# Optimization experiments

Measured on AMD Instinct MI355X. Metric: run time of the kernel, lower is better.

## Reference

```python
import jax, jax.numpy as jnp
import numpy as np


def _conv1d(x, w, b):
    # x: [N, C_in, L], w: [C_out, C_in, K], padding=1 (SAME for K=3)
    y = jax.lax.conv_general_dilated(
        x, w, window_strides=(1,), padding=[(1, 1)],
        dimension_numbers=('NCH', 'OIH', 'NCH'))
    return y + b[None, :, None]


def _pharse_shift(I, r):
    # Faithful vectorized form of the original scalar loop:
    #   New[i, 0, j] = I[i, j % r, j // r];  all other output channels stay zero.
    a, b, c = I.shape
    row0 = jnp.transpose(I[:, :r, :], (0, 2, 1)).reshape(a, c * r)  # interleave channels
    New = jnp.zeros((a, b // r, c * r), dtype=I.dtype)
    return New.at[:, 0, :].set(row0)


def setup_inputs() -> dict:
    key = jax.random.key(0)
    k1, k2, k3, k4, k5 = jax.random.split(key, 5)
    B, C, L = 32, 64, 16384
    x = jax.random.normal(k1, (B, C, L), dtype=jnp.float32)
    # Conv1d(channels, channels, 3) params, PyTorch-style uniform init scale
    s1 = 1.0 / np.sqrt(C * 3)
    w1 = jax.random.uniform(k2, (C, C, 3), minval=-s1, maxval=s1, dtype=jnp.float32)
    b1 = jax.random.uniform(k3, (C,), minval=-s1, maxval=s1, dtype=jnp.float32)
    # Conv1d(channels, 4, 3) params (up_block22)
    w2 = jax.random.uniform(k4, (4, C, 3), minval=-s1, maxval=s1, dtype=jnp.float32)
    b2 = jax.random.uniform(k5, (4,), minval=-s1, maxval=s1, dtype=jnp.float32)
    return {"x": x, "w1": w1, "b1": b1, "w2": w2, "b2": b2, "sc": 4}


def reference(x, w1, b1, w2, b2, sc):
    assert sc in (2, 4)
    h = jax.nn.relu(_conv1d(x, w1, b1))   # up_block1: Conv1d(C,C,3)+ReLU
    h = jax.nn.relu(_conv1d(h, w2, b2))   # up_block22: Conv1d(C,4,3)+ReLU  [B,4,L]
    return _pharse_shift(h, sc)           # [B, 4//sc, L*sc]
```

## Files before the change

### kernel.cpp

```cpp
#include <hip/hip_runtime.h>
#include <hip/hip_bf16.h>


#define CC 64
#define LL 16384
#define NBATCH 32
#define TL 128
#define NTILE 128
#define XROWS 146
#define PITCH 128

typedef short short8 __attribute__((ext_vector_type(8)));
typedef float f32x4 __attribute__((ext_vector_type(4)));

__device__ __forceinline__ unsigned pk2(float a, float b) {
    unsigned short lo = __builtin_bit_cast(unsigned short, __float2bfloat16(a));
    unsigned short hi = __builtin_bit_cast(unsigned short, __float2bfloat16(b));
    return (unsigned)lo | ((unsigned)hi << 16);
}

__global__ void repack_weights(const float* __restrict__ w1,
                               const float* __restrict__ w2,
                               unsigned short* __restrict__ wp) {
    int i = blockIdx.x * 256 + threadIdx.x;
    if (i < 12288) {
        int kk = i >> 12;
        int rem = i & 4095;
        int co = rem >> 6;
        int ci = rem & 63;
        wp[i] = __builtin_bit_cast(unsigned short, __float2bfloat16(w1[(co * 64 + ci) * 3 + kk]));
    }
    if (i < 3072) {
        int kk = i >> 10;
        int rem = i & 1023;
        int oc = rem >> 6;
        int ci = rem & 63;
        float v = (oc < 4) ? w2[(oc * 64 + ci) * 3 + kk] : 0.0f;
        wp[12288 + i] = __builtin_bit_cast(unsigned short, __float2bfloat16(v));
    }
}

__global__ __launch_bounds__(256, 4)
void fused_upsample_mfma(const float* __restrict__ x,
                         const float* __restrict__ b1,
                         const float* __restrict__ b2,
                         const unsigned short* __restrict__ wp,
                         float* __restrict__ out) {
    __shared__ __align__(16) char lds[(XROWS + 2 + 144) * PITCH];
    char* const xs = lds;
    char* const hs = lds + (XROWS + 2) * PITCH;

    const int bid = blockIdx.x;
    const int swz = (bid & 7) * 512 + (bid >> 3);
    const int t   = swz & (NTILE - 1);
    const int bb  = swz >> 7;

    const int tid  = threadIdx.x;
    const int lane = tid & 63;
    const int wave = tid >> 6;
    const int lr   = lane & 15;
    const int lg   = lane >> 4;

    {
        const int sc  = tid & 15;
        const int scg = tid >> 4;
        const long base0 = (long)(bb * CC + scg * 4) * LL;
        const int g0 = t * TL - 2;
        const bool interior = (t > 0) && (t < NTILE - 1);

        if (interior) {
            #pragma unroll
            for (int it = 0; it < 5; ++it) {
                int r = it * 32 + sc * 2;
                if (it < 4 || r < XROWS) {
                    float2 v0 = *(const float2*)(x + base0 + g0 + r);
                    float2 v1 = *(const float2*)(x + base0 + LL + g0 + r);
                    float2 v2 = *(const float2*)(x + base0 + 2 * LL + g0 + r);
                    float2 v3 = *(const float2*)(x + base0 + 3 * LL + g0 + r);
                    int byteA = (r * PITCH + scg * 8) ^ ((r & 7) << 4);
                    int byteB = ((r + 1) * PITCH + scg * 8) ^ (((r + 1) & 7) << 4);
                    *(uint2*)(xs + byteA) = make_uint2(pk2(v0.x, v1.x), pk2(v2.x, v3.x));
                    *(uint2*)(xs + byteB) = make_uint2(pk2(v0.y, v1.y), pk2(v2.y, v3.y));
                }
            }
        } else {
            #pragma unroll
            for (int it = 0; it < 5; ++it) {
                int r = it * 32 + sc * 2;
                if (it < 4 || r < XROWS) {
                    int ga = g0 + r, gb = g0 + r + 1;
                    bool oa = (unsigned)ga < (unsigned)LL;
                    bool ob = (unsigned)gb < (unsigned)LL;
                    float2 v[4];
                    #pragma unroll
                    for (int u = 0; u < 4; ++u) {
                        v[u].x = oa ? x[base0 + (long)u * LL + ga] : 0.f;
                        v[u].y = ob ? x[base0 + (long)u * LL + gb] : 0.f;
                    }
                    int byteA = (r * PITCH + scg * 8) ^ ((r & 7) << 4);
                    int byteB = ((r + 1) * PITCH + scg * 8) ^ (((r + 1) & 7) << 4);
                    *(uint2*)(xs + byteA) = make_uint2(pk2(v[0].x, v[1].x), pk2(v[2].x, v[3].x));
                    *(uint2*)(xs + byteB) = make_uint2(pk2(v[0].y, v[1].y), pk2(v[2].y, v[3].y));
                }
            }
        }
    }
    __syncthreads();

    {
        short8 A1[3][2];
        #pragma unroll
        for (int k = 0; k < 3; ++k)
            #pragma unroll
            for (int kc = 0; kc < 2; ++kc)
                A1[k][kc] = *(const short8*)(wp + ((k * 64 + wave * 16 + lr) * 64 + kc * 32 + lg * 8));
        const f32x4 bias1 = *(const f32x4*)(b1 + wave * 16 + lg * 4);

        #pragma unroll 1
        for (int i = 0; i < 9; ++i) {
            f32x4 acc = bias1;
            #pragma unroll
            for (int k = 0; k < 3; ++k) {
                int row = 16 * i + lr + k;
                #pragma unroll
                for (int kc = 0; kc < 2; ++kc) {
                    int byte = (row * PITCH + kc * 64 + lg * 16) ^ ((row & 7) << 4);
                    short8 Bf = *(const short8*)(xs + byte);
                    acc = __builtin_amdgcn_mfma_f32_16x16x32_bf16(A1[k][kc], Bf, acc, 0, 0, 0);
                }
            }
            int p  = 16 * i - 1 + lr;
            int hp = t * TL + p;
            bool inr = (unsigned)hp < (unsigned)LL;
            float r0 = inr ? fmaxf(acc[0], 0.f) : 0.f;
            float r1 = inr ? fmaxf(acc[1], 0.f) : 0.f;
            float r2 = inr ? fmaxf(acc[2], 0.f) : 0.f;
            float r3 = inr ? fmaxf(acc[3], 0.f) : 0.f;
            int hrow = 16 * i + lr;
            int byte = (hrow * PITCH + wave * 32 + lg * 8) ^ ((hrow & 7) << 4);
            *(uint2*)(hs + byte) = make_uint2(pk2(r0, r1), pk2(r2, r3));
        }
    }
    __syncthreads();

    {
        short8 A2[3][2];
        #pragma unroll
        for (int k = 0; k < 3; ++k)
            #pragma unroll
            for (int kc = 0; kc < 2; ++kc)
                A2[k][kc] = *(const short8*)(wp + 12288 + ((k * 16 + lr) * 64 + kc * 32 + lg * 8));
        const f32x4 bias2v = *(const f32x4*)(b2);
        const f32x4 zero4 = {0.f, 0.f, 0.f, 0.f};
        const f32x4 acc2init = (lg == 0) ? bias2v : zero4;

        #pragma unroll
        for (int s = 0; s < 2; ++s) {
            int p0 = 16 * (wave * 2 + s);
            f32x4 acc = acc2init;
            #pragma unroll
            for (int k = 0; k < 3; ++k) {
                int row = p0 + lr + k;
                #pragma unroll
                for (int kc = 0; kc < 2; ++kc) {
                    int byte = (row * PITCH + kc * 64 + lg * 16) ^ ((row & 7) << 4);
                    short8 Bf = *(const short8*)(hs + byte);
                    acc = __builtin_amdgcn_mfma_f32_16x16x32_bf16(A2[k][kc], Bf, acc, 0, 0, 0);
                }
            }
            if (lane < 16) {
                f32x4 o;
                o[0] = fmaxf(acc[0], 0.f);
                o[1] = fmaxf(acc[1], 0.f);
                o[2] = fmaxf(acc[2], 0.f);
                o[3] = fmaxf(acc[3], 0.f);
                *(f32x4*)(out + (long)bb * (LL * 4) + (t * TL + p0 + lane) * 4) = o;
            }
        }
    }
}

extern "C" void kernel_launch(void* const* d_in, const int* in_sizes, int n_in,
                              void* d_out, int out_size, void* d_ws, size_t ws_size,
                              hipStream_t stream) {
    const float* x  = (const float*)d_in[0];
    const float* w1 = (const float*)d_in[1];
    const float* b1 = (const float*)d_in[2];
    const float* w2 = (const float*)d_in[3];
    const float* b2 = (const float*)d_in[4];
    float* out = (float*)d_out;
    unsigned short* wp = (unsigned short*)d_ws;

    repack_weights<<<48, 256, 0, stream>>>(w1, w2, wp);
    fused_upsample_mfma<<<NTILE * NBATCH, 256, 0, stream>>>(x, b1, b2, wp, out);
}
```

Before: 51.47 us.

## Pipeline tiles across two 256-thread groups with staggered load/conv phases

Each block now has 512 threads split into two roles. Each role owns its own LDS buffer and processes two tiles, so a block covers four consecutive tiles. The roles run a three-phase schedule (load, conv1, conv2) offset by one step, so one group's global loads overlap the other group's MFMA work. This adds a block-wide barrier every step and doubles LDS per block, which may lower the number of resident blocks per CU, and the grid shrinks to a quarter of its former size.

After: 66.42 us. +29.0%, slower.

```diff
diff --git a/kernel.cpp b/kernel.cpp
--- a/kernel.cpp
+++ b/kernel.cpp
@@ -7,8 +7,10 @@
 #define NBATCH 32
 #define TL 128
 #define NTILE 128
+#define NT 4
 #define XROWS 146
 #define PITCH 128
+#define LDSBUF ((XROWS + 2 + 144) * PITCH)
 
 typedef short short8 __attribute__((ext_vector_type(8)));
 typedef float f32x4 __attribute__((ext_vector_type(4)));
@@ -40,143 +42,151 @@
     }
 }
 
-__global__ __launch_bounds__(256, 4)
+__global__ __launch_bounds__(512, 4)
 void fused_upsample_mfma(const float* __restrict__ x,
                          const float* __restrict__ b1,
                          const float* __restrict__ b2,
                          const unsigned short* __restrict__ wp,
                          float* __restrict__ out) {
-    __shared__ __align__(16) char lds[(XROWS + 2 + 144) * PITCH];
-    char* const xs = lds;
-    char* const hs = lds + (XROWS + 2) * PITCH;
+    __shared__ __align__(16) char lds[2 * LDSBUF];
 
     const int bid = blockIdx.x;
-    const int swz = (bid & 7) * 512 + (bid >> 3);
-    const int t   = swz & (NTILE - 1);
-    const int bb  = swz >> 7;
-
-    const int tid  = threadIdx.x;
-    const int lane = tid & 63;
-    const int wave = tid >> 6;
-    const int lr   = lane & 15;
-    const int lg   = lane >> 4;
-
-    {
-        const int sc  = tid & 15;
-        const int scg = tid >> 4;
-        const long base0 = (long)(bb * CC + scg * 4) * LL;
-        const int g0 = t * TL - 2;
-        const bool interior = (t > 0) && (t < NTILE - 1);
-
-        if (interior) {
-            #pragma unroll
-            for (int it = 0; it < 5; ++it) {
-                int r = it * 32 + sc * 2;
-                if (it < 4 || r < XROWS) {
-                    float2 v0 = *(const float2*)(x + base0 + g0 + r);
-                    float2 v1 = *(const float2*)(x + base0 + LL + g0 + r);
-                    float2 v2 = *(const float2*)(x + base0 + 2 * LL + g0 + r);
-                    float2 v3 = *(const float2*)(x + base0 + 3 * LL + g0 + r);
-                    int byteA = (r * PITCH + scg * 8) ^ ((r & 7) << 4);
-                    int byteB = ((r + 1) * PITCH + scg * 8) ^ (((r + 1) & 7) << 4);
-                    *(uint2*)(xs + byteA) = make_uint2(pk2(v0.x, v1.x), pk2(v2.x, v3.x));
-                    *(uint2*)(xs + byteB) = make_uint2(pk2(v0.y, v1.y), pk2(v2.y, v3.y));
+    const int swz = (bid & 7) * 128 + (bid >> 3);
+    const int bb  = swz >> 5;
+    const int t0  = (swz & 31) * NT;
+
+    const int tid   = threadIdx.x;
+    const int role  = tid >> 8;
+    const int ltid  = tid & 255;
+    const int lane  = ltid & 63;
+    const int gwave = ltid >> 6;
+    const int lr    = lane & 15;
+    const int lg    = lane >> 4;
+
+    char* const xs = lds + role * LDSBUF;
+    char* const hs = xs + (XROWS + 2) * PITCH;
+
+    const int sc  = ltid & 15;
+    const int scg = ltid >> 4;
+    const long base0 = (long)(bb * CC + scg * 4) * LL;
+
+    const int NSTEP = 3 * (NT / 2) + 1;
+    for (int s = 0; s < NSTEP; ++s) {
+        const int sg = role ? s - 1 : s;
+        const bool active = (sg >= 0) && ((sg / 3) < NT / 2);
+        if (active) {
+            const int ph = sg % 3;
+            const int t  = t0 + (sg / 3) * 2 + role;
+
+            if (ph == 0) {
+                const int g0 = t * TL - 2;
+                const bool interior = (t > 0) && (t < NTILE - 1);
+                if (interior) {
+                    #pragma unroll
+                    for (int it = 0; it < 5; ++it) {
+                        int r = it * 32 + sc * 2;
+                        if (it < 4 || r < XROWS) {
+                            float2 v0 = *(const float2*)(x + base0 + g0 + r);
+                            float2 v1 = *(const float2*)(x + base0 + LL + g0 + r);
+                            float2 v2 = *(const float2*)(x + base0 + 2 * LL + g0 + r);
+                            float2 v3 = *(const float2*)(x + base0 + 3 * LL + g0 + r);
+                            int byteA = (r * PITCH + scg * 8) ^ ((r & 7) << 4);
+                            int byteB = ((r + 1) * PITCH + scg * 8) ^ (((r + 1) & 7) << 4);
+                            *(uint2*)(xs + byteA) = make_uint2(pk2(v0.x, v1.x), pk2(v2.x, v3.x));
+                            *(uint2*)(xs + byteB) = make_uint2(pk2(v0.y, v1.y), pk2(v2.y, v3.y));
+                        }
+                    }
+                } else {
+                    #pragma unroll
+                    for (int it = 0; it < 5; ++it) {
+                        int r = it * 32 + sc * 2;
+                        if (it < 4 || r < XROWS) {
+                            int ga = g0 + r, gb = g0 + r + 1;
+                            bool oa = (unsigned)ga < (unsigned)LL;
+                            bool ob = (unsigned)gb < (unsigned)LL;
+                            float2 v[4];
+                            #pragma unroll
+                            for (int u = 0; u < 4; ++u) {
+                                v[u].x = oa ? x[base0 + (long)u * LL + ga] : 0.f;
+                                v[u].y = ob ? x[base0 + (long)u * LL + gb] : 0.f;
+                            }
+                            int byteA = (r * PITCH + scg * 8) ^ ((r & 7) << 4);
+                            int byteB = ((r + 1) * PITCH + scg * 8) ^ (((r + 1) & 7) << 4);
+                            *(uint2*)(xs + byteA) = make_uint2(pk2(v[0].x, v[1].x), pk2(v[2].x, v[3].x));
+                            *(uint2*)(xs + byteB) = make_uint2(pk2(v[0].y, v[1].y), pk2(v[2].y, v[3].y));
+                        }
+                    }
                 }
-            }
-        } else {
-            #pragma unroll
-            for (int it = 0; it < 5; ++it) {
-                int r = it * 32 + sc * 2;
-                if (it < 4 || r < XROWS) {
-                    int ga = g0 + r, gb = g0 + r + 1;
-                    bool oa = (unsigned)ga < (unsigned)LL;
-                    bool ob = (unsigned)gb < (unsigned)LL;
-                    float2 v[4];
-                    #pragma unroll
-                    for (int u = 0; u < 4; ++u) {
-                        v[u].x = oa ? x[base0 + (long)u * LL + ga] : 0.f;
-                        v[u].y = ob ? x[base0 + (long)u * LL + gb] : 0.f;
-                    }
-                    int byteA = (r * PITCH + scg * 8) ^ ((r & 7) << 4);
-                    int byteB = ((r + 1) * PITCH + scg * 8) ^ (((r + 1) & 7) << 4);
-                    *(uint2*)(xs + byteA) = make_uint2(pk2(v[0].x, v[1].x), pk2(v[2].x, v[3].x));
-                    *(uint2*)(xs + byteB) = make_uint2(pk2(v[0].y, v[1].y), pk2(v[2].y, v[3].y));
+            } else if (ph == 1) {
+                short8 A1[3][2];
+                #pragma unroll
+                for (int k = 0; k < 3; ++k)
+                    #pragma unroll
+                    for (int kc = 0; kc < 2; ++kc)
+                        A1[k][kc] = *(const short8*)(wp + ((k * 64 + gwave * 16 + lr) * 64 + kc * 32 + lg * 8));
+                const f32x4 bias1 = *(const f32x4*)(b1 + gwave * 16 + lg * 4);
+
+                #pragma unroll 1
+                for (int i = 0; i < 9; ++i) {
+                    f32x4 acc = bias1;
+                    #pragma unroll
+                    for (int k = 0; k < 3; ++k) {
+                        int row = 16 * i + lr + k;
+                        #pragma unroll
+                        for (int kc = 0; kc < 2; ++kc) {
+                            int byte = (row * PITCH + kc * 64 + lg * 16) ^ ((row & 7) << 4);
+                            short8 Bf = *(const short8*)(xs + byte);
+                            acc = __builtin_amdgcn_mfma_f32_16x16x32_bf16(A1[k][kc], Bf, acc, 0, 0, 0);
+                        }
+                    }
+                    int p  = 16 * i - 1 + lr;
+                    int hp = t * TL + p;
+                    bool inr = (unsigned)hp < (unsigned)LL;
+                    float r0 = inr ? fmaxf(acc[0], 0.f) : 0.f;
+                    float r1 = inr ? fmaxf(acc[1], 0.f) : 0.f;
+                    float r2 = inr ? fmaxf(acc[2], 0.f) : 0.f;
+                    float r3 = inr ? fmaxf(acc[3], 0.f) : 0.f;
+                    int hrow = 16 * i + lr;
+                    int byte = (hrow * PITCH + gwave * 32 + lg * 8) ^ ((hrow & 7) << 4);
+                    *(uint2*)(hs + byte) = make_uint2(pk2(r0, r1), pk2(r2, r3));
+                }
+            } else {
+                short8 A2[3][2];
+                #pragma unroll
+                for (int k = 0; k < 3; ++k)
+                    #pragma unroll
+                    for (int kc = 0; kc < 2; ++kc)
+                        A2[k][kc] = *(const short8*)(wp + 12288 + ((k * 16 + lr) * 64 + kc * 32 + lg * 8));
+                const f32x4 bias2v = *(const f32x4*)(b2);
+                const f32x4 zero4 = {0.f, 0.f, 0.f, 0.f};
+                const f32x4 acc2init = (lg == 0) ? bias2v : zero4;
+
+                #pragma unroll
+                for (int ss = 0; ss < 2; ++ss) {
+                    int p0 = 16 * (gwave * 2 + ss);
+                    f32x4 acc = acc2init;
+                    #pragma unroll
+                    for (int k = 0; k < 3; ++k) {
+                        int row = p0 + lr + k;
+                        #pragma unroll
+                        for (int kc = 0; kc < 2; ++kc) {
+                            int byte = (row * PITCH + kc * 64 + lg * 16) ^ ((row & 7) << 4);
+                            short8 Bf = *(const short8*)(hs + byte);
+                            acc = __builtin_amdgcn_mfma_f32_16x16x32_bf16(A2[k][kc], Bf, acc, 0, 0, 0);
+                        }
+                    }
+                    if (lane < 16) {
+                        f32x4 o;
+                        o[0] = fmaxf(acc[0], 0.f);
+                        o[1] = fmaxf(acc[1], 0.f);
+                        o[2] = fmaxf(acc[2], 0.f);
+                        o[3] = fmaxf(acc[3], 0.f);
+                        *(f32x4*)(out + (long)bb * (LL * 4) + (t * TL + p0 + lane) * 4) = o;
+                    }
                 }
             }
         }
-    }
-    __syncthreads();
-
-    {
-        short8 A1[3][2];
-        #pragma unroll
-        for (int k = 0; k < 3; ++k)
-            #pragma unroll
-            for (int kc = 0; kc < 2; ++kc)
-                A1[k][kc] = *(const short8*)(wp + ((k * 64 + wave * 16 + lr) * 64 + kc * 32 + lg * 8));
-        const f32x4 bias1 = *(const f32x4*)(b1 + wave * 16 + lg * 4);
-
-        #pragma unroll 1
-        for (int i = 0; i < 9; ++i) {
-            f32x4 acc = bias1;
-            #pragma unroll
-            for (int k = 0; k < 3; ++k) {
-                int row = 16 * i + lr + k;
-                #pragma unroll
-                for (int kc = 0; kc < 2; ++kc) {
-                    int byte = (row * PITCH + kc * 64 + lg * 16) ^ ((row & 7) << 4);
-                    short8 Bf = *(const short8*)(xs + byte);
-                    acc = __builtin_amdgcn_mfma_f32_16x16x32_bf16(A1[k][kc], Bf, acc, 0, 0, 0);
-                }
-            }
-            int p  = 16 * i - 1 + lr;
-            int hp = t * TL + p;
-            bool inr = (unsigned)hp < (unsigned)LL;
-            float r0 = inr ? fmaxf(acc[0], 0.f) : 0.f;
-            float r1 = inr ? fmaxf(acc[1], 0.f) : 0.f;
-            float r2 = inr ? fmaxf(acc[2], 0.f) : 0.f;
-            float r3 = inr ? fmaxf(acc[3], 0.f) : 0.f;
-            int hrow = 16 * i + lr;
-            int byte = (hrow * PITCH + wave * 32 + lg * 8) ^ ((hrow & 7) << 4);
-            *(uint2*)(hs + byte) = make_uint2(pk2(r0, r1), pk2(r2, r3));
-        }
-    }
-    __syncthreads();
-
-    {
-        short8 A2[3][2];
-        #pragma unroll
-        for (int k = 0; k < 3; ++k)
-            #pragma unroll
-            for (int kc = 0; kc < 2; ++kc)
-                A2[k][kc] = *(const short8*)(wp + 12288 + ((k * 16 + lr) * 64 + kc * 32 + lg * 8));
-        const f32x4 bias2v = *(const f32x4*)(b2);
-        const f32x4 zero4 = {0.f, 0.f, 0.f, 0.f};
-        const f32x4 acc2init = (lg == 0) ? bias2v : zero4;
-
-        #pragma unroll
-        for (int s = 0; s < 2; ++s) {
-            int p0 = 16 * (wave * 2 + s);
-            f32x4 acc = acc2init;
-            #pragma unroll
-            for (int k = 0; k < 3; ++k) {
-                int row = p0 + lr + k;
-                #pragma unroll
-                for (int kc = 0; kc < 2; ++kc) {
-                    int byte = (row * PITCH + kc * 64 + lg * 16) ^ ((row & 7) << 4);
-                    short8 Bf = *(const short8*)(hs + byte);
-                    acc = __builtin_amdgcn_mfma_f32_16x16x32_bf16(A2[k][kc], Bf, acc, 0, 0, 0);
-                }
-            }
-            if (lane < 16) {
-                f32x4 o;
-                o[0] = fmaxf(acc[0], 0.f);
-                o[1] = fmaxf(acc[1], 0.f);
-                o[2] = fmaxf(acc[2], 0.f);
-                o[3] = fmaxf(acc[3], 0.f);
-                *(f32x4*)(out + (long)bb * (LL * 4) + (t * TL + p0 + lane) * 4) = o;
-            }
-        }
+        __syncthreads();
     }
 }
 
@@ -192,5 +202,5 @@
     unsigned short* wp = (unsigned short*)d_ws;
 
     repack_weights<<<48, 256, 0, stream>>>(w1, w2, wp);
-    fused_upsample_mfma<<<NTILE * NBATCH, 256, 0, stream>>>(x, b1, b2, wp, out);
-}
+    fused_upsample_mfma<<<(NTILE / NT) * NBATCH, 512, 0, stream>>>(x, b1, b2, wp, out);
+}
```
